# Kernel tuning notes

Measured on AMD Instinct MI355X. Metric: run time of the kernel, lower is better.

Reference implementation:

```python
import jax, jax.numpy as jnp
import numpy as np
import math

HIDDEN = 256
NUM_GAUSSIANS = 64
NUM_FILTERS = 256
CUTOFF = 1.0
COSINE_OFFSET = 0.0
N_NODES = 10000
N_EDGES = 320000


def ssp(x):
    # shifted softplus: softplus(x) - log(2)
    return jax.nn.softplus(x) - jnp.log(2.0).astype(x.dtype)


def setup_inputs() -> dict:
    key = jax.random.key(0)
    ks = jax.random.split(key, 12)

    def xavier(k, fan_out, fan_in):
        a = math.sqrt(6.0 / (fan_in + fan_out))
        return jax.random.uniform(k, (fan_out, fan_in), jnp.float32, -a, a)

    x = jax.random.normal(ks[0], (N_NODES, HIDDEN), jnp.float32)
    ji_pairs = jax.random.randint(ks[1], (2, N_EDGES), 0, N_NODES, jnp.int64)
    e_ji = jax.random.uniform(ks[2], (N_EDGES,), jnp.float32)  # distances in [0, cutoff)
    e_ji_basis = jax.random.normal(ks[3], (N_EDGES, NUM_GAUSSIANS), jnp.float32)

    return {
        "x": x,
        "ji_pairs": ji_pairs,
        "e_ji": e_ji,
        "e_ji_basis": e_ji_basis,
        # filter_nn: Linear(G->F), ssp, Linear(F->F)
        "fw1": xavier(ks[4], NUM_FILTERS, NUM_GAUSSIANS),
        "fb1": jnp.zeros((NUM_FILTERS,), jnp.float32),
        "fw2": xavier(ks[5], NUM_FILTERS, NUM_FILTERS),
        "fb2": jnp.zeros((NUM_FILTERS,), jnp.float32),
        # CFConv linears
        "w1": xavier(ks[6], NUM_FILTERS, HIDDEN),            # linear1, no bias
        "w2": xavier(ks[7], HIDDEN, NUM_FILTERS),            # linear2
        "b2": jnp.zeros((HIDDEN,), jnp.float32),
        # linear3
        "w3": xavier(ks[8], HIDDEN, HIDDEN),
        "b3": jnp.zeros((HIDDEN,), jnp.float32),
    }


def reference(x, ji_pairs, e_ji, e_ji_basis, fw1, fb1, fw2, fb2, w1, w2, b2, w3, b3):
    pi = jnp.asarray(math.pi, x.dtype)
    # cosine cutoff: C = 0.25 * (cos((e - off) * pi / (cutoff - off)) + 1)
    C = 0.25 * (jnp.cos((e_ji - COSINE_OFFSET) * pi / (CUTOFF - COSINE_OFFSET)) + 1.0)
    # filter network on edge RBF features: [E, F]
    W = ssp(e_ji_basis @ fw1.T + fb1) @ fw2.T + fb2
    W = W * C[:, None]
    # linear1 (no bias): [N, F]
    h = x @ w1.T
    # message: x_j * W, gathered from source nodes ji_pairs[0]
    src, dst = ji_pairs[0], ji_pairs[1]
    msg = h[src] * W                                   # [E, F]
    agg = jax.ops.segment_sum(msg, dst, num_segments=x.shape[0])  # [N, F]
    # linear2
    out = agg @ w2.T + b2
    # interaction block tail: act + linear3
    out = ssp(out) @ w3.T + b3
    return out
```

## Files before the change

### kernel.cpp

```cpp
#include <hip/hip_runtime.h>
#include <hip/hip_bf16.h>

typedef __bf16 bf16_t;
typedef float f32x4 __attribute__((ext_vector_type(4)));
typedef __bf16 bf16x8 __attribute__((ext_vector_type(8)));

#define NNODES 10000
#define NEDGES 320000
#define NPAD   10048
#define NPB    8
#define NBLK   (NPAD / NPB)

#define OFF_AGG   256
#define OFF_JIN   (OFF_AGG  + (size_t)NPAD * 256 * 4)
#define OFF_HIST  (OFF_JIN  + (size_t)2 * NEDGES * 4)
#define OFF_CUR   (OFF_HIST + 10240 * 4)
#define OFF_CSR   (OFF_CUR  + 10240 * 4)
#define OFF_PERM  (OFF_CSR  + 10240 * 4)
#define OFF_SRCS  (OFF_PERM + (size_t)NEDGES * 4)
#define OFF_DSTS  (OFF_SRCS + (size_t)NEDGES * 4)
#define OFF_CES   (OFF_DSTS + (size_t)NEDGES * 4)
#define OFF_CE    (OFF_CES  + (size_t)NEDGES * 4)
#define OFF_WB    (OFF_CE   + (size_t)NEDGES * 4)
#define FW1B 0
#define FW2B 16384
#define W1B  81920
#define W2B  147456
#define W3B  212992
#define FB1B 278528
#define FB2B 278784
#define B2B  279040
#define B3B  279296
#define WBN  279552
#define WS_NEED (OFF_WB + (size_t)WBN * 2)
#define OFF_BASC  ((WS_NEED + 255) & ~(size_t)255)
#define WS_NEED_BIG (OFF_BASC + (size_t)NEDGES * 64 * 2)

__device__ __forceinline__ float ssp_f(float v) {
    return fmaxf(v, 0.f) + __logf(1.f + __expf(-fabsf(v))) - 0.69314718055994531f;
}
__device__ __forceinline__ f32x4 mfma16(bf16x8 a, bf16x8 b, f32x4 c) {
    return __builtin_amdgcn_mfma_f32_16x16x32_bf16(a, b, c, 0, 0, 0);
}
template<bool ISB>
__device__ __forceinline__ bf16x8 ld8(const void* p, size_t off) {
    if constexpr (ISB) return *(const bf16x8*)((const bf16_t*)p + off);
    else {
        const float* f = (const float*)p + off;
        f32x4 lo = *(const f32x4*)f, hi = *(const f32x4*)(f + 4);
        bf16x8 r;
        for (int j = 0; j < 4; ++j) { r[j] = (bf16_t)lo[j]; r[j + 4] = (bf16_t)hi[j]; }
        return r;
    }
}
__device__ __forceinline__ bf16x8 ld8r(bool isb, const void* p, size_t off) {
    if (isb) return *(const bf16x8*)((const bf16_t*)p + off);
    const float* f = (const float*)p + off;
    f32x4 lo = *(const f32x4*)f, hi = *(const f32x4*)(f + 4);
    bf16x8 r;
    for (int j = 0; j < 4; ++j) { r[j] = (bf16_t)lo[j]; r[j + 4] = (bf16_t)hi[j]; }
    return r;
}
template<bool ISB>
__device__ __forceinline__ void st1(void* p, size_t off, float v) {
    if constexpr (ISB) ((bf16_t*)p)[off] = (bf16_t)v;
    else               ((float*)p)[off] = v;
}
__device__ __forceinline__ float ld1r(bool isb, const void* p, size_t off) {
    return isb ? (float)((const bf16_t*)p)[off] : ((const float*)p)[off];
}

__global__ __launch_bounds__(256) void detect_kernel(
    const void* __restrict__ x, const int* __restrict__ jraw,
    int* __restrict__ flags, int* __restrict__ hist)
{
    __shared__ int cnt, hi;
    if (threadIdx.x == 0) { cnt = 0; hi = 0; }
    __syncthreads();
    const unsigned short* xw = (const unsigned short*)x;
    int local = 0;
    for (int i = threadIdx.x; i < 2048; i += 256) {
        unsigned int e = (xw[2 * i] >> 7) & 0xFF;
        if (e >= 100 && e <= 141) local++;
    }
    atomicAdd(&cnt, local);
    int v = 0;
    for (int i = threadIdx.x; i < 1024; i += 256) v |= jraw[2 * i + 1];
    if (v != 0) atomicOr(&hi, 1);
    for (int i = threadIdx.x; i < 10240; i += 256) hist[i] = 0;
    __syncthreads();
    if (threadIdx.x == 0) { flags[0] = (cnt > 1024) ? 1 : 0; flags[1] = (hi == 0) ? 1 : 0; }
}

__global__ __launch_bounds__(256) void prep_kernel(
    const int* __restrict__ raw, const int* __restrict__ flags,
    const void* __restrict__ e_ji, const void* __restrict__ basis,
    const void* fw1, const void* fb1, const void* fw2, const void* fb2,
    const void* w1, const void* w2, const void* b2, const void* w3, const void* b3,
    int* __restrict__ jin, int* __restrict__ hist, float* __restrict__ ce,
    bf16_t* __restrict__ wb, bf16_t* __restrict__ basc, int doconv)
{
    const bool is64 = (flags[1] != 0);
    const bool isb  = (flags[0] != 0);
    const int gid = blockIdx.x * 256 + threadIdx.x;
    if (gid < 2 * NEDGES) {
        int iv = is64 ? raw[2 * gid] : raw[gid];
        iv = iv < 0 ? 0 : (iv >= NNODES ? NNODES - 1 : iv);
        jin[gid] = iv;
        if (gid >= NEDGES) atomicAdd(&hist[iv], 1);
    }
    if (gid < NEDGES)
        ce[gid] = 0.25f * (cosf(3.14159265358979f * ld1r(isb, e_ji, gid)) + 1.0f);
    if (gid < WBN) {
        int g = gid; const void* s; int so;
        if      (g < FW2B) { s = fw1; so = g - FW1B; }
        else if (g < W1B)  { s = fw2; so = g - FW2B; }
        else if (g < W2B)  { s = w1;  so = g - W1B; }
        else if (g < W3B)  { s = w2;  so = g - W2B; }
        else if (g < FB1B) { s = w3;  so = g - W3B; }
        else if (g < FB2B) { s = fb1; so = g - FB1B; }
        else if (g < B2B)  { s = fb2; so = g - FB2B; }
        else if (g < B3B)  { s = b2;  so = g - B2B; }
        else               { s = b3;  so = g - B3B; }
        wb[gid] = (bf16_t)ld1r(isb, s, so);
    }
    if (doconv) {
        const int nv = NEDGES * 64 / 8;
        for (int i = gid; i < nv; i += gridDim.x * 256)
            ((bf16x8*)basc)[i] = ld8r(isb, basis, (size_t)i * 8);
    }
}

__global__ __launch_bounds__(256) void scan_kernel(
    const int* __restrict__ hist, int* __restrict__ cur, int* __restrict__ csr)
{
    __shared__ int s[256];
    const int t = threadIdx.x;
    int loc[40]; int sum = 0;
    const int base = t * 40;
    for (int j = 0; j < 40; ++j) {
        int i = base + j;
        loc[j] = (i < NNODES) ? hist[i] : 0;
        sum += loc[j];
    }
    s[t] = sum; __syncthreads();
    for (int off = 1; off < 256; off <<= 1) {
        int v = (t >= off) ? s[t - off] : 0;
        __syncthreads();
        if (t >= off) s[t] += v;
        __syncthreads();
    }
    int pre = (t == 0) ? 0 : s[t - 1];
    for (int j = 0; j < 40; ++j) {
        int i = base + j;
        cur[i] = pre;
        csr[i] = pre;
        pre += loc[j];
    }
}

__global__ __launch_bounds__(256) void scatter_kernel(
    const int* __restrict__ jin, const float* __restrict__ ce,
    int* __restrict__ cur, int* __restrict__ perm,
    int* __restrict__ src_s, int* __restrict__ dst_s, float* __restrict__ ce_s)
{
    int e = blockIdx.x * 256 + threadIdx.x;
    if (e < NEDGES) {
        int d = jin[NEDGES + e];
        int pos = atomicAdd(&cur[d], 1);
        perm[pos]  = e;
        src_s[pos] = jin[e];
        dst_s[pos] = d;
        ce_s[pos]  = ce[e];
    }
}

template<bool ISB>
__global__ __launch_bounds__(256, 2) void h_gemm_kernel(
    const void* __restrict__ x, const bf16_t* __restrict__ wb,
    bf16_t* __restrict__ h, const int* __restrict__ flags)
{
    if ((flags[0] != 0) != ISB) return;
    const bf16_t* w1b = wb + W1B;
    const int w = threadIdx.x >> 6, L = threadIdx.x & 63;
    const int lane16 = L & 15, quad = L >> 4;
    const int nb = blockIdx.x * 64, cb = w * 64;
    f32x4 acc[4][4] = {};
    for (int kc = 0; kc < 8; ++kc) {
        const int ko = kc * 32 + quad * 8;
        bf16x8 af[4], bfr[4];
        for (int mt = 0; mt < 4; ++mt) {
            int row = nb + mt * 16 + lane16;
            if (row >= NNODES) row = NNODES - 1;
            af[mt] = ld8<ISB>(x, (size_t)row * 256 + ko);
        }
        for (int nt = 0; nt < 4; ++nt)
            bfr[nt] = *(const bf16x8*)(w1b + (size_t)(cb + nt * 16 + lane16) * 256 + ko);
        for (int mt = 0; mt < 4; ++mt)
            for (int nt = 0; nt < 4; ++nt)
                acc[mt][nt] = mfma16(af[mt], bfr[nt], acc[mt][nt]);
    }
    for (int mt = 0; mt < 4; ++mt)
        for (int r = 0; r < 4; ++r) {
            int row = nb + mt * 16 + quad * 4 + r;
            if (row < NNODES)
                for (int nt = 0; nt < 4; ++nt)
                    h[(size_t)row * 256 + cb + nt * 16 + lane16] = (bf16_t)acc[mt][nt][r];
        }
}

template<bool ISB, bool CONV>
__global__ __launch_bounds__(256, 3) void edge_kernel(
    const void* __restrict__ basis, const int* __restrict__ csr,
    const int* __restrict__ perm, const int* __restrict__ src_s,
    const int* __restrict__ dst_s, const float* __restrict__ ce_s,
    const bf16_t* __restrict__ wb, const bf16_t* __restrict__ h,
    float* __restrict__ agg, const int* __restrict__ flags)
{
    if (!CONV && (flags[0] != 0) != ISB) return;
    __shared__ bf16_t T[64][264];
    __shared__ float G[NPB][260];
    __shared__ int sperm[64], ssrc[64], snrow[64];
    __shared__ float sce[64];
    const int tid = threadIdx.x;
    const int w = tid >> 6, L = tid & 63;
    const int lane16 = L & 15, quad = L >> 4;
    const int cb = w * 64;
    const int nbase  = blockIdx.x * NPB;
    const int estart = csr[nbase];
    const int eend   = csr[nbase + NPB];

    for (int i = tid; i < NPB * 260; i += 256) (&G[0][0])[i] = 0.f;

    const bf16_t* fw1b = wb + FW1B;
    const bf16_t* fw2b = wb + FW2B;
    float fb1v[4], fb2v[4];
    for (int nt = 0; nt < 4; ++nt) {
        fb1v[nt] = (float)wb[FB1B + cb + nt * 16 + lane16];
        fb2v[nt] = (float)wb[FB2B + cb + nt * 16 + lane16];
    }

    const int hrow = tid >> 2, hseg = tid & 3;

    for (int e0 = estart & ~63; e0 < eend; e0 += 64) {
        __syncthreads();
        {
            int g = tid >> 6, i = tid & 63;
            int e = e0 + i;
            bool valid = (e >= estart) && (e < eend);
            int ee = valid ? e : estart;
            if      (g == 0) sperm[i] = perm[ee];
            else if (g == 1) ssrc[i] = src_s[ee];
            else if (g == 2) {
                int nr = dst_s[ee] - nbase;
                snrow[i] = nr < 0 ? 0 : (nr > NPB - 1 ? NPB - 1 : nr);
            }
            else sce[i] = valid ? ce_s[ee] : 0.f;
        }
        __syncthreads();

        bf16x8 hreg[8];
        {
            const bf16_t* hs = h + (size_t)ssrc[hrow] * 256 + hseg * 64;
            #pragma unroll
            for (int j = 0; j < 8; ++j) hreg[j] = ((const bf16x8*)hs)[j];
        }

        int prow[4];
        for (int mt = 0; mt < 4; ++mt) prow[mt] = sperm[mt * 16 + lane16];

        f32x4 acc1[4][4] = {};
        for (int kc = 0; kc < 2; ++kc) {
            const int ko = kc * 32 + quad * 8;
            bf16x8 af[4], bfr[4];
            for (int mt = 0; mt < 4; ++mt)
                af[mt] = ld8<CONV ? true : ISB>(basis, (size_t)prow[mt] * 64 + ko);
            for (int nt = 0; nt < 4; ++nt)
                bfr[nt] = *(const bf16x8*)(fw1b + (size_t)(cb + nt * 16 + lane16) * 64 + ko);
            for (int mt = 0; mt < 4; ++mt)
                for (int nt = 0; nt < 4; ++nt)
                    acc1[mt][nt] = mfma16(af[mt], bfr[nt], acc1[mt][nt]);
        }
        for (int nt = 0; nt < 4; ++nt) {
            int col = cb + nt * 16 + lane16;
            for (int mt = 0; mt < 4; ++mt)
                for (int r = 0; r < 4; ++r)
                    T[mt * 16 + quad * 4 + r][col] = (bf16_t)ssp_f(acc1[mt][nt][r] + fb1v[nt]);
        }
        __syncthreads();

        f32x4 acc2[4][4] = {};
        for (int kc = 0; kc < 8; ++kc) {
            const int ko = kc * 32 + quad * 8;
            bf16x8 af[4], bfr[4];
            for (int mt = 0; mt < 4; ++mt)
                af[mt] = *(const bf16x8*)(&T[mt * 16 + lane16][ko]);
            for (int nt = 0; nt < 4; ++nt)
                bfr[nt] = *(const bf16x8*)(fw2b + (size_t)(cb + nt * 16 + lane16) * 256 + ko);
            for (int mt = 0; mt < 4; ++mt)
                for (int nt = 0; nt < 4; ++nt)
                    acc2[mt][nt] = mfma16(af[mt], bfr[nt], acc2[mt][nt]);
        }
        __syncthreads();

        {
            bf16_t* dp = &T[hrow][hseg * 64];
            #pragma unroll
            for (int j = 0; j < 8; ++j) ((bf16x8*)dp)[j] = hreg[j];
        }
        __syncthreads();

        float run[4] = {0, 0, 0, 0};
        int curn = -1;
        for (int mt = 0; mt < 4; ++mt)
            for (int r = 0; r < 4; ++r) {
                int row = mt * 16 + quad * 4 + r;
                int nr = snrow[row];
                if (nr != curn) {
                    if (curn >= 0)
                        for (int nt = 0; nt < 4; ++nt)
                            atomicAdd(&G[curn][cb + nt * 16 + lane16], run[nt]);
                    curn = nr;
                    run[0] = run[1] = run[2] = run[3] = 0.f;
                }
                float cv = sce[row];
                for (int nt = 0; nt < 4; ++nt) {
                    int col = cb + nt * 16 + lane16;
                    run[nt] += (acc2[mt][nt][r] + fb2v[nt]) * cv * (float)T[row][col];
                }
            }
        if (curn >= 0)
            for (int nt = 0; nt < 4; ++nt)
                atomicAdd(&G[curn][cb + nt * 16 + lane16], run[nt]);
    }
    __syncthreads();

    for (int n = 0; n < NPB; ++n)
        agg[(size_t)(nbase + n) * 256 + tid] = G[n][tid];
}

template<bool ISB>
__global__ __launch_bounds__(256, 2) void out_kernel(
    const float* __restrict__ agg, const bf16_t* __restrict__ wb,
    void* __restrict__ out, const int* __restrict__ flags)
{
    if ((flags[0] != 0) != ISB) return;
    const bf16_t* w2b = wb + W2B;
    const bf16_t* w3b = wb + W3B;
    __shared__ bf16_t U[64][264];
    const int w = threadIdx.x >> 6, L = threadIdx.x & 63;
    const int lane16 = L & 15, quad = L >> 4;
    const int nb = blockIdx.x * 64, cb = w * 64;

    f32x4 acc[4][4] = {};
    for (int kc = 0; kc < 8; ++kc) {
        const int ko = kc * 32 + quad * 8;
        bf16x8 af[4], bfr[4];
        for (int mt = 0; mt < 4; ++mt) {
            int row = nb + mt * 16 + lane16;
            const float* p = agg + (size_t)row * 256 + ko;
            f32x4 lo = *(const f32x4*)p, hi = *(const f32x4*)(p + 4);
            bf16x8 a;
            for (int j = 0; j < 4; ++j) { a[j] = (bf16_t)lo[j]; a[j + 4] = (bf16_t)hi[j]; }
            af[mt] = a;
        }
        for (int nt = 0; nt < 4; ++nt)
            bfr[nt] = *(const bf16x8*)(w2b + (size_t)(cb + nt * 16 + lane16) * 256 + ko);
        for (int mt = 0; mt < 4; ++mt)
            for (int nt = 0; nt < 4; ++nt)
                acc[mt][nt] = mfma16(af[mt], bfr[nt], acc[mt][nt]);
    }
    for (int nt = 0; nt < 4; ++nt) {
        int col = cb + nt * 16 + lane16;
        float bias = (float)wb[B2B + col];
        for (int mt = 0; mt < 4; ++mt)
            for (int r = 0; r < 4; ++r)
                U[mt * 16 + quad * 4 + r][col] = (bf16_t)ssp_f(acc[mt][nt][r] + bias);
    }
    __syncthreads();

    f32x4 acc2[4][4] = {};
    for (int kc = 0; kc < 8; ++kc) {
        const int ko = kc * 32 + quad * 8;
        bf16x8 af[4], bfr[4];
        for (int mt = 0; mt < 4; ++mt)
            af[mt] = *(const bf16x8*)(&U[mt * 16 + lane16][ko]);
        for (int nt = 0; nt < 4; ++nt)
            bfr[nt] = *(const bf16x8*)(w3b + (size_t)(cb + nt * 16 + lane16) * 256 + ko);
        for (int mt = 0; mt < 4; ++mt)
            for (int nt = 0; nt < 4; ++nt)
                acc2[mt][nt] = mfma16(af[mt], bfr[nt], acc2[mt][nt]);
    }
    for (int mt = 0; mt < 4; ++mt)
        for (int r = 0; r < 4; ++r) {
            int row = nb + mt * 16 + quad * 4 + r;
            if (row < NNODES)
                for (int nt = 0; nt < 4; ++nt) {
                    int col = cb + nt * 16 + lane16;
                    st1<ISB>(out, (size_t)row * 256 + col,
                             acc2[mt][nt][r] + (float)wb[B3B + col]);
                }
        }
}

extern "C" void kernel_launch(void* const* d_in, const int* in_sizes, int n_in,
                              void* d_out, int out_size, void* d_ws, size_t ws_size,
                              hipStream_t stream) {
    const void* x     = d_in[0];
    const int*  ji    = (const int*)d_in[1];
    const void* e_ji  = d_in[2];
    const void* basis = d_in[3];
    const void* fw1   = d_in[4];
    const void* fb1   = d_in[5];
    const void* fw2   = d_in[6];
    const void* fb2   = d_in[7];
    const void* w1    = d_in[8];
    const void* w2    = d_in[9];
    const void* b2    = d_in[10];
    const void* w3    = d_in[11];
    const void* b3    = d_in[12];

    if (ws_size < WS_NEED) return;
    const bool bigws = ws_size >= WS_NEED_BIG;

    char* W = (char*)d_ws;
    int*    flags = (int*)W;
    float*  agg   = (float*)(W + OFF_AGG);
    int*    jin   = (int*)(W + OFF_JIN);
    int*    hist  = (int*)(W + OFF_HIST);
    int*    cur   = (int*)(W + OFF_CUR);
    int*    csr   = (int*)(W + OFF_CSR);
    int*    perm  = (int*)(W + OFF_PERM);
    int*    src_s = (int*)(W + OFF_SRCS);
    int*    dst_s = (int*)(W + OFF_DSTS);
    float*  ce_s  = (float*)(W + OFF_CES);
    float*  ce    = (float*)(W + OFF_CE);
    bf16_t* wb    = (bf16_t*)(W + OFF_WB);
    bf16_t* basc  = (bf16_t*)(W + OFF_BASC);
    bf16_t* h     = (bf16_t*)d_out;

    detect_kernel<<<1, 256, 0, stream>>>(x, ji, flags, hist);
    prep_kernel<<<2500, 256, 0, stream>>>(ji, flags, e_ji, basis, fw1, fb1, fw2, fb2,
                                          w1, w2, b2, w3, b3, jin, hist, ce, wb,
                                          basc, bigws ? 1 : 0);
    scan_kernel<<<1, 256, 0, stream>>>(hist, cur, csr);
    scatter_kernel<<<1250, 256, 0, stream>>>(jin, ce, cur, perm, src_s, dst_s, ce_s);
    h_gemm_kernel<true ><<<157, 256, 0, stream>>>(x, wb, h, flags);
    h_gemm_kernel<false><<<157, 256, 0, stream>>>(x, wb, h, flags);
    if (bigws) {
        edge_kernel<true, true><<<NBLK, 256, 0, stream>>>(basc, csr, perm, src_s, dst_s, ce_s, wb, h, agg, flags);
    } else {
        edge_kernel<true,  false><<<NBLK, 256, 0, stream>>>(basis, csr, perm, src_s, dst_s, ce_s, wb, h, agg, flags);
        edge_kernel<false, false><<<NBLK, 256, 0, stream>>>(basis, csr, perm, src_s, dst_s, ce_s, wb, h, agg, flags);
    }
    out_kernel<true ><<<157, 256, 0, stream>>>(agg, wb, d_out, flags);
    out_kernel<false><<<157, 256, 0, stream>>>(agg, wb, d_out, flags);
}
```

Measured before the change: 582.5 us.

## Software-pipeline edge kernel with async h gather to LDS and basis prefetch

Restructures the edge kernel into a two-stage software pipeline. Next-chunk metadata and basis rows are prefetched into registers while the current chunk is computed, and gathered h rows are loaded straight into a dedicated LDS buffer with global_load_lds instead of passing through registers. One barrier phase is dropped. The bf16/fp32 template duplicates of h_gemm and out_kernel are merged into runtime-branch versions, removing extra launches, and loops get unroll pragmas. The extra 32KB LDS buffer and more registers lower occupancy (launch bounds 3 to 2 blocks), which could offset the overlap gains.

```diff
diff --git a/kernel.cpp b/kernel.cpp
--- a/kernel.cpp
+++ b/kernel.cpp
@@ -1,5 +1,6 @@
 #include <hip/hip_runtime.h>
 #include <hip/hip_bf16.h>
+#include <stdint.h>
 
 typedef __bf16 bf16_t;
 typedef float f32x4 __attribute__((ext_vector_type(4)));
@@ -49,6 +50,7 @@
         const float* f = (const float*)p + off;
         f32x4 lo = *(const f32x4*)f, hi = *(const f32x4*)(f + 4);
         bf16x8 r;
+        #pragma unroll
         for (int j = 0; j < 4; ++j) { r[j] = (bf16_t)lo[j]; r[j + 4] = (bf16_t)hi[j]; }
         return r;
     }
@@ -58,16 +60,22 @@
     const float* f = (const float*)p + off;
     f32x4 lo = *(const f32x4*)f, hi = *(const f32x4*)(f + 4);
     bf16x8 r;
+    #pragma unroll
     for (int j = 0; j < 4; ++j) { r[j] = (bf16_t)lo[j]; r[j + 4] = (bf16_t)hi[j]; }
     return r;
 }
-template<bool ISB>
-__device__ __forceinline__ void st1(void* p, size_t off, float v) {
-    if constexpr (ISB) ((bf16_t*)p)[off] = (bf16_t)v;
-    else               ((float*)p)[off] = v;
+__device__ __forceinline__ void st1r(bool isb, void* p, size_t off, float v) {
+    if (isb) ((bf16_t*)p)[off] = (bf16_t)v;
+    else     ((float*)p)[off] = v;
 }
 __device__ __forceinline__ float ld1r(bool isb, const void* p, size_t off) {
     return isb ? (float)((const bf16_t*)p)[off] : ((const float*)p)[off];
+}
+__device__ __forceinline__ void gld_lds16(const bf16_t* g, bf16_t* l) {
+    __builtin_amdgcn_global_load_lds(
+        (const __attribute__((address_space(1))) unsigned int*)g,
+        (__attribute__((address_space(3))) unsigned int*)l,
+        16, 0, 0);
 }
 
 __global__ __launch_bounds__(256) void detect_kernel(
@@ -138,6 +146,7 @@
     const int t = threadIdx.x;
     int loc[40]; int sum = 0;
     const int base = t * 40;
+    #pragma unroll
     for (int j = 0; j < 40; ++j) {
         int i = base + j;
         loc[j] = (i < NNODES) ? hist[i] : 0;
@@ -151,6 +160,7 @@
         __syncthreads();
     }
     int pre = (t == 0) ? 0 : s[t - 1];
+    #pragma unroll
     for (int j = 0; j < 40; ++j) {
         int i = base + j;
         cur[i] = pre;
@@ -175,53 +185,62 @@
     }
 }
 
-template<bool ISB>
 __global__ __launch_bounds__(256, 2) void h_gemm_kernel(
     const void* __restrict__ x, const bf16_t* __restrict__ wb,
     bf16_t* __restrict__ h, const int* __restrict__ flags)
 {
-    if ((flags[0] != 0) != ISB) return;
+    const bool isb = (flags[0] != 0);
     const bf16_t* w1b = wb + W1B;
     const int w = threadIdx.x >> 6, L = threadIdx.x & 63;
     const int lane16 = L & 15, quad = L >> 4;
     const int nb = blockIdx.x * 64, cb = w * 64;
     f32x4 acc[4][4] = {};
+    #pragma unroll
     for (int kc = 0; kc < 8; ++kc) {
         const int ko = kc * 32 + quad * 8;
         bf16x8 af[4], bfr[4];
+        #pragma unroll
         for (int mt = 0; mt < 4; ++mt) {
             int row = nb + mt * 16 + lane16;
             if (row >= NNODES) row = NNODES - 1;
-            af[mt] = ld8<ISB>(x, (size_t)row * 256 + ko);
-        }
+            af[mt] = ld8r(isb, x, (size_t)row * 256 + ko);
+        }
+        #pragma unroll
         for (int nt = 0; nt < 4; ++nt)
             bfr[nt] = *(const bf16x8*)(w1b + (size_t)(cb + nt * 16 + lane16) * 256 + ko);
+        #pragma unroll
         for (int mt = 0; mt < 4; ++mt)
+            #pragma unroll
             for (int nt = 0; nt < 4; ++nt)
                 acc[mt][nt] = mfma16(af[mt], bfr[nt], acc[mt][nt]);
     }
+    #pragma unroll
     for (int mt = 0; mt < 4; ++mt)
+        #pragma unroll
         for (int r = 0; r < 4; ++r) {
             int row = nb + mt * 16 + quad * 4 + r;
             if (row < NNODES)
+                #pragma unroll
                 for (int nt = 0; nt < 4; ++nt)
                     h[(size_t)row * 256 + cb + nt * 16 + lane16] = (bf16_t)acc[mt][nt][r];
         }
 }
 
-template<bool ISB, bool CONV>
-__global__ __launch_bounds__(256, 3) void edge_kernel(
+template<bool ISB>
+__global__ __launch_bounds__(256, 2) void edge_pipe_kernel(
     const void* __restrict__ basis, const int* __restrict__ csr,
     const int* __restrict__ perm, const int* __restrict__ src_s,
     const int* __restrict__ dst_s, const float* __restrict__ ce_s,
     const bf16_t* __restrict__ wb, const bf16_t* __restrict__ h,
-    float* __restrict__ agg, const int* __restrict__ flags)
-{
-    if (!CONV && (flags[0] != 0) != ISB) return;
+    float* __restrict__ agg, const int* __restrict__ flags, int guard)
+{
+    if (guard >= 0 && ((flags[0] != 0) != (guard == 1))) return;
     __shared__ bf16_t T[64][264];
+    __shared__ bf16_t Hs[64 * 256];
     __shared__ float G[NPB][260];
-    __shared__ int sperm[64], ssrc[64], snrow[64];
-    __shared__ float sce[64];
+    __shared__ int   smeta[2][3][64];
+    __shared__ float smce[2][64];
+
     const int tid = threadIdx.x;
     const int w = tid >> 6, L = tid & 63;
     const int lane16 = L & 15, quad = L >> 4;
@@ -235,116 +254,162 @@
     const bf16_t* fw1b = wb + FW1B;
     const bf16_t* fw2b = wb + FW2B;
     float fb1v[4], fb2v[4];
+    #pragma unroll
     for (int nt = 0; nt < 4; ++nt) {
         fb1v[nt] = (float)wb[FB1B + cb + nt * 16 + lane16];
         fb2v[nt] = (float)wb[FB2B + cb + nt * 16 + lane16];
     }
 
-    const int hrow = tid >> 2, hseg = tid & 3;
-
-    for (int e0 = estart & ~63; e0 < eend; e0 += 64) {
-        __syncthreads();
+    const int e0beg = estart & ~63;
+    const int nsub  = (eend - e0beg + 63) >> 6;
+    const int esafe = (estart < NEDGES) ? estart : NEDGES - 1;
+
+    {
+        int e = e0beg + L;
+        bool valid = (e >= estart) && (e < eend);
+        int ee = valid ? e : esafe;
+        if      (w == 0) smeta[0][0][L] = perm[ee];
+        else if (w == 1) smeta[0][1][L] = src_s[ee];
+        else if (w == 2) {
+            int nr = dst_s[ee] - nbase;
+            smeta[0][2][L] = nr < 0 ? 0 : (nr > NPB - 1 ? NPB - 1 : nr);
+        }
+        else smce[0][L] = valid ? ce_s[ee] : 0.f;
+    }
+    __syncthreads();
+
+    bf16x8 bcur[8];
+    #pragma unroll
+    for (int mt = 0; mt < 4; ++mt) {
+        int prow = smeta[0][0][mt * 16 + lane16];
+        #pragma unroll
+        for (int kc = 0; kc < 2; ++kc)
+            bcur[kc * 4 + mt] = ld8<ISB>(basis, (size_t)prow * 64 + kc * 32 + quad * 8);
+    }
+
+    for (int si = 0; si < nsub; ++si) {
+        const int buf = si & 1;
+        int miv = 0; float mfv = 0.f;
         {
-            int g = tid >> 6, i = tid & 63;
-            int e = e0 + i;
+            int sn = (si + 1 < nsub) ? si + 1 : si;
+            int e = e0beg + sn * 64 + L;
             bool valid = (e >= estart) && (e < eend);
-            int ee = valid ? e : estart;
-            if      (g == 0) sperm[i] = perm[ee];
-            else if (g == 1) ssrc[i] = src_s[ee];
-            else if (g == 2) {
+            int ee = valid ? e : esafe;
+            if      (w == 0) miv = perm[ee];
+            else if (w == 1) miv = src_s[ee];
+            else if (w == 2) {
                 int nr = dst_s[ee] - nbase;
-                snrow[i] = nr < 0 ? 0 : (nr > NPB - 1 ? NPB - 1 : nr);
+                miv = nr < 0 ? 0 : (nr > NPB - 1 ? NPB - 1 : nr);
             }
-            else sce[i] = valid ? ce_s[ee] : 0.f;
-        }
-        __syncthreads();
-
-        bf16x8 hreg[8];
-        {
-            const bf16_t* hs = h + (size_t)ssrc[hrow] * 256 + hseg * 64;
-            #pragma unroll
-            for (int j = 0; j < 8; ++j) hreg[j] = ((const bf16x8*)hs)[j];
-        }
-
-        int prow[4];
-        for (int mt = 0; mt < 4; ++mt) prow[mt] = sperm[mt * 16 + lane16];
+            else mfv = valid ? ce_s[ee] : 0.f;
+        }
 
         f32x4 acc1[4][4] = {};
+        #pragma unroll
         for (int kc = 0; kc < 2; ++kc) {
-            const int ko = kc * 32 + quad * 8;
-            bf16x8 af[4], bfr[4];
+            bf16x8 bfr[4];
+            #pragma unroll
+            for (int nt = 0; nt < 4; ++nt)
+                bfr[nt] = *(const bf16x8*)(fw1b + (size_t)(cb + nt * 16 + lane16) * 64 + kc * 32 + quad * 8);
+            #pragma unroll
             for (int mt = 0; mt < 4; ++mt)
-                af[mt] = ld8<CONV ? true : ISB>(basis, (size_t)prow[mt] * 64 + ko);
-            for (int nt = 0; nt < 4; ++nt)
-                bfr[nt] = *(const bf16x8*)(fw1b + (size_t)(cb + nt * 16 + lane16) * 64 + ko);
-            for (int mt = 0; mt < 4; ++mt)
+                #pragma unroll
                 for (int nt = 0; nt < 4; ++nt)
-                    acc1[mt][nt] = mfma16(af[mt], bfr[nt], acc1[mt][nt]);
-        }
+                    acc1[mt][nt] = mfma16(bcur[kc * 4 + mt], bfr[nt], acc1[mt][nt]);
+        }
+        #pragma unroll
         for (int nt = 0; nt < 4; ++nt) {
             int col = cb + nt * 16 + lane16;
+            #pragma unroll
             for (int mt = 0; mt < 4; ++mt)
+                #pragma unroll
                 for (int r = 0; r < 4; ++r)
                     T[mt * 16 + quad * 4 + r][col] = (bf16_t)ssp_f(acc1[mt][nt][r] + fb1v[nt]);
         }
+        if (w == 3) smce[buf ^ 1][L] = mfv;
+        else        smeta[buf ^ 1][w][L] = miv;
         __syncthreads();
 
+        #pragma unroll
+        for (int j = 0; j < 8; ++j) {
+            int row = w * 16 + j * 2 + (L >> 5);
+            int srcrow = smeta[buf][1][row];
+            gld_lds16(h + (size_t)srcrow * 256 + (L & 31) * 8,
+                      &Hs[w * 4096 + j * 512]);
+        }
+        bf16x8 bnext[8];
+        #pragma unroll
+        for (int mt = 0; mt < 4; ++mt) {
+            int prow = smeta[buf ^ 1][0][mt * 16 + lane16];
+            #pragma unroll
+            for (int kc = 0; kc < 2; ++kc)
+                bnext[kc * 4 + mt] = ld8<ISB>(basis, (size_t)prow * 64 + kc * 32 + quad * 8);
+        }
+
         f32x4 acc2[4][4] = {};
+        #pragma unroll
         for (int kc = 0; kc < 8; ++kc) {
             const int ko = kc * 32 + quad * 8;
             bf16x8 af[4], bfr[4];
+            #pragma unroll
             for (int mt = 0; mt < 4; ++mt)
                 af[mt] = *(const bf16x8*)(&T[mt * 16 + lane16][ko]);
+            #pragma unroll
             for (int nt = 0; nt < 4; ++nt)
                 bfr[nt] = *(const bf16x8*)(fw2b + (size_t)(cb + nt * 16 + lane16) * 256 + ko);
+            #pragma unroll
             for (int mt = 0; mt < 4; ++mt)
+                #pragma unroll
                 for (int nt = 0; nt < 4; ++nt)
                     acc2[mt][nt] = mfma16(af[mt], bfr[nt], acc2[mt][nt]);
         }
         __syncthreads();
 
-        {
-            bf16_t* dp = &T[hrow][hseg * 64];
-            #pragma unroll
-            for (int j = 0; j < 8; ++j) ((bf16x8*)dp)[j] = hreg[j];
-        }
-        __syncthreads();
-
-        float run[4] = {0, 0, 0, 0};
+        float run[4] = {0.f, 0.f, 0.f, 0.f};
         int curn = -1;
+        #pragma unroll
         for (int mt = 0; mt < 4; ++mt)
+            #pragma unroll
             for (int r = 0; r < 4; ++r) {
                 int row = mt * 16 + quad * 4 + r;
-                int nr = snrow[row];
+                int nr = smeta[buf][2][row];
                 if (nr != curn) {
-                    if (curn >= 0)
+                    if (curn >= 0) {
+                        #pragma unroll
                         for (int nt = 0; nt < 4; ++nt)
                             atomicAdd(&G[curn][cb + nt * 16 + lane16], run[nt]);
+                    }
                     curn = nr;
-                    run[0] = run[1] = run[2] = run[3] = 0.f;
+                    #pragma unroll
+                    for (int nt = 0; nt < 4; ++nt) run[nt] = 0.f;
                 }
-                float cv = sce[row];
+                float cv = smce[buf][row];
+                #pragma unroll
                 for (int nt = 0; nt < 4; ++nt) {
                     int col = cb + nt * 16 + lane16;
-                    run[nt] += (acc2[mt][nt][r] + fb2v[nt]) * cv * (float)T[row][col];
+                    run[nt] += (acc2[mt][nt][r] + fb2v[nt]) * cv * (float)Hs[row * 256 + col];
                 }
             }
-        if (curn >= 0)
-            for (int nt = 0; nt < 4; ++nt)
-                atomicAdd(&G[curn][cb + nt * 16 + lane16], run[nt]);
+        #pragma unroll
+        for (int nt = 0; nt < 4; ++nt)
+            atomicAdd(&G[curn][cb + nt * 16 + lane16], run[nt]);
+        __syncthreads();
+
+        #pragma unroll
+        for (int k = 0; k < 8; ++k) bcur[k] = bnext[k];
     }
     __syncthreads();
 
+    #pragma unroll
     for (int n = 0; n < NPB; ++n)
         agg[(size_t)(nbase + n) * 256 + tid] = G[n][tid];
 }
 
-template<bool ISB>
 __global__ __launch_bounds__(256, 2) void out_kernel(
     const float* __restrict__ agg, const bf16_t* __restrict__ wb,
     void* __restrict__ out, const int* __restrict__ flags)
 {
-    if ((flags[0] != 0) != ISB) return;
+    const bool isb = (flags[0] != 0);
     const bf16_t* w2b = wb + W2B;
     const bf16_t* w3b = wb + W3B;
     __shared__ bf16_t U[64][264];
@@ -353,52 +418,69 @@
     const int nb = blockIdx.x * 64, cb = w * 64;
 
     f32x4 acc[4][4] = {};
+    #pragma unroll
     for (int kc = 0; kc < 8; ++kc) {
         const int ko = kc * 32 + quad * 8;
         bf16x8 af[4], bfr[4];
+        #pragma unroll
         for (int mt = 0; mt < 4; ++mt) {
             int row = nb + mt * 16 + lane16;
             const float* p = agg + (size_t)row * 256 + ko;
             f32x4 lo = *(const f32x4*)p, hi = *(const f32x4*)(p + 4);
             bf16x8 a;
+            #pragma unroll
             for (int j = 0; j < 4; ++j) { a[j] = (bf16_t)lo[j]; a[j + 4] = (bf16_t)hi[j]; }
             af[mt] = a;
         }
+        #pragma unroll
         for (int nt = 0; nt < 4; ++nt)
             bfr[nt] = *(const bf16x8*)(w2b + (size_t)(cb + nt * 16 + lane16) * 256 + ko);
+        #pragma unroll
         for (int mt = 0; mt < 4; ++mt)
+            #pragma unroll
             for (int nt = 0; nt < 4; ++nt)
                 acc[mt][nt] = mfma16(af[mt], bfr[nt], acc[mt][nt]);
     }
+    #pragma unroll
     for (int nt = 0; nt < 4; ++nt) {
         int col = cb + nt * 16 + lane16;
         float bias = (float)wb[B2B + col];
+        #pragma unroll
         for (int mt = 0; mt < 4; ++mt)
+            #pragma unroll
             for (int r = 0; r < 4; ++r)
                 U[mt * 16 + quad * 4 + r][col] = (bf16_t)ssp_f(acc[mt][nt][r] + bias);
     }
     __syncthreads();
 
     f32x4 acc2[4][4] = {};
+    #pragma unroll
     for (int kc = 0; kc < 8; ++kc) {
         const int ko = kc * 32 + quad * 8;
         bf16x8 af[4], bfr[4];
+        #pragma unroll
         for (int mt = 0; mt < 4; ++mt)
             af[mt] = *(const bf16x8*)(&U[mt * 16 + lane16][ko]);
+        #pragma unroll
         for (int nt = 0; nt < 4; ++nt)
             bfr[nt] = *(const bf16x8*)(w3b + (size_t)(cb + nt * 16 + lane16) * 256 + ko);
+        #pragma unroll
         for (int mt = 0; mt < 4; ++mt)
+            #pragma unroll
             for (int nt = 0; nt < 4; ++nt)
                 acc2[mt][nt] = mfma16(af[mt], bfr[nt], acc2[mt][nt]);
     }
+    #pragma unroll
     for (int mt = 0; mt < 4; ++mt)
+        #pragma unroll
         for (int r = 0; r < 4; ++r) {
             int row = nb + mt * 16 + quad * 4 + r;
             if (row < NNODES)
+                #pragma unroll
                 for (int nt = 0; nt < 4; ++nt) {
                     int col = cb + nt * 16 + lane16;
-                    st1<ISB>(out, (size_t)row * 256 + col,
-                             acc2[mt][nt][r] + (float)wb[B3B + col]);
+                    st1r(isb, out, (size_t)row * 256 + col,
+                         acc2[mt][nt][r] + (float)wb[B3B + col]);
                 }
         }
 }
@@ -445,14 +527,15 @@
                                           basc, bigws ? 1 : 0);
     scan_kernel<<<1, 256, 0, stream>>>(hist, cur, csr);
     scatter_kernel<<<1250, 256, 0, stream>>>(jin, ce, cur, perm, src_s, dst_s, ce_s);
-    h_gemm_kernel<true ><<<157, 256, 0, stream>>>(x, wb, h, flags);
-    h_gemm_kernel<false><<<157, 256, 0, stream>>>(x, wb, h, flags);
+    h_gemm_kernel<<<157, 256, 0, stream>>>(x, wb, h, flags);
     if (bigws) {
-        edge_kernel<true, true><<<NBLK, 256, 0, stream>>>(basc, csr, perm, src_s, dst_s, ce_s, wb, h, agg, flags);
+        edge_pipe_kernel<true><<<NBLK, 256, 0, stream>>>(basc, csr, perm, src_s, dst_s,
+                                                         ce_s, wb, h, agg, flags, -1);
     } else {
-        edge_kernel<true,  false><<<NBLK, 256, 0, stream>>>(basis, csr, perm, src_s, dst_s, ce_s, wb, h, agg, flags);
-        edge_kernel<false, false><<<NBLK, 256, 0, stream>>>(basis, csr, perm, src_s, dst_s, ce_s, wb, h, agg, flags);
-    }
-    out_kernel<true ><<<157, 256, 0, stream>>>(agg, wb, d_out, flags);
-    out_kernel<false><<<157, 256, 0, stream>>>(agg, wb, d_out, flags);
-}
+        edge_pipe_kernel<true ><<<NBLK, 256, 0, stream>>>(basis, csr, perm, src_s, dst_s,
+                                                          ce_s, wb, h, agg, flags, 1);
+        edge_pipe_kernel<false><<<NBLK, 256, 0, stream>>>(basis, csr, perm, src_s, dst_s,
+                                                          ce_s, wb, h, agg, flags, 0);
+    }
+    out_kernel<<<157, 256, 0, stream>>>(agg, wb, d_out, flags);
+}
```

New measurement: 602.9 us. 3.5% more time.
